# Kernel optimization log

Hardware: AMD Instinct MI355X
Metric: run time of the kernel (lower is better)

The kernel has to match this reference:

```python
import jax, jax.numpy as jnp
import numpy as np

H = 1024        # hidden_size
NH = 16         # num_heads
HD = H // NH    # head_dim
NS = 3          # num_strata


def setup_inputs() -> dict:
    key = jax.random.key(0)
    ks = jax.random.split(key, 12)
    s = 1.0 / np.sqrt(H)
    inp = {
        "hidden_states": jax.random.normal(ks[0], (2, 2048, H), dtype=jnp.float32),
        "Wq": jax.random.uniform(ks[1], (H, H), minval=-s, maxval=s, dtype=jnp.float32),
        "bq": jax.random.uniform(ks[2], (H,), minval=-s, maxval=s, dtype=jnp.float32),
        "Wk": jax.random.uniform(ks[3], (H, H), minval=-s, maxval=s, dtype=jnp.float32),
        "bk": jax.random.uniform(ks[4], (H,), minval=-s, maxval=s, dtype=jnp.float32),
        "Wv": jax.random.uniform(ks[5], (H, H), minval=-s, maxval=s, dtype=jnp.float32),
        "bv": jax.random.uniform(ks[6], (H,), minval=-s, maxval=s, dtype=jnp.float32),
        "Ws": jax.random.uniform(ks[7], (NS, H, H), minval=-s, maxval=s, dtype=jnp.float32),
        "bs": jax.random.uniform(ks[8], (NS, H), minval=-s, maxval=s, dtype=jnp.float32),
        "Wo": jax.random.uniform(ks[9], (H, H), minval=-s, maxval=s, dtype=jnp.float32),
        "bo": jax.random.uniform(ks[10], (H,), minval=-s, maxval=s, dtype=jnp.float32),
    }
    return inp


def reference(hidden_states, Wq, bq, Wk, bk, Wv, bv, Ws, bs, Wo, bo):
    B, S, _ = hidden_states.shape
    # torch nn.Linear: y = x @ W.T + b
    q = hidden_states @ Wq.T + bq
    k = hidden_states @ Wk.T + bk
    v = hidden_states @ Wv.T + bv
    # [B, NH, S, HD]
    q = q.reshape(B, S, NH, HD).transpose(0, 2, 1, 3)
    k = k.reshape(B, S, NH, HD).transpose(0, 2, 1, 3)
    v = v.reshape(B, S, NH, HD).transpose(0, 2, 1, 3)
    scores = jnp.einsum('bhqd,bhkd->bhqk', q, k) / jnp.sqrt(jnp.float32(HD))
    attn = jax.nn.softmax(scores, axis=-1)
    out = jnp.einsum('bhqk,bhkd->bhqd', attn, v)
    attn_output = out.transpose(0, 2, 1, 3).reshape(B, S, H)
    # stratum projections, averaged: [NS, B, S, H] -> mean over strata
    strata = jnp.einsum('bsh,ngh->nbsg', attn_output, Ws) + bs[:, None, None, :]
    enhanced = strata.mean(axis=0)
    output = enhanced @ Wo.T + bo
    return output
```

## Files before the change

### kernel.cpp

```cpp
#include <hip/hip_runtime.h>
#include <stdint.h>

typedef __attribute__((ext_vector_type(8))) short short8;
typedef __attribute__((ext_vector_type(4))) short short4v;
typedef __attribute__((ext_vector_type(4))) float f32x4;
typedef __attribute__((ext_vector_type(2))) unsigned int u32x2;
typedef unsigned int u32;
typedef const __attribute__((address_space(1))) u32* gas_ptr;
typedef __attribute__((address_space(3))) u32* las_ptr;

#define QSCALE 0.18033688011112042f

__device__ inline short f2bf(float x) {
    u32 u = __float_as_uint(x);
    u = u + 0x7FFFu + ((u >> 16) & 1u);
    return (short)(u >> 16);
}
__device__ inline void gload16(const void* g, const void* l) {
    __builtin_amdgcn_global_load_lds((gas_ptr)g, (las_ptr)l, 16, 0, 0);
}

__global__ __launch_bounds__(256) void prep(const float* __restrict__ X,
                                            const float* __restrict__ Wq,
                                            const float* __restrict__ Wk,
                                            const float* __restrict__ Wv,
                                            const float* __restrict__ Wo,
                                            const float* __restrict__ Ws,
                                            const float* __restrict__ bs,
                                            const float* __restrict__ bo,
                                            short* __restrict__ Xb,
                                            short* __restrict__ Wcat,
                                            short* __restrict__ Wob,
                                            short* __restrict__ WmT,
                                            float* __restrict__ bc) {
    __shared__ short T[64][65];
    const int tid = threadIdx.x;
    const int bid = blockIdx.x;
    if (bid < 8192) {
        const float* src;
        short* dst;
        int rel;
        if (bid < 4096)      { src = X;  dst = Xb;                rel = bid; }
        else if (bid < 5120) { src = Wq; dst = Wcat;              rel = bid - 4096; }
        else if (bid < 6144) { src = Wk; dst = Wcat + (1 << 20);  rel = bid - 5120; }
        else if (bid < 7168) { src = Wv; dst = Wcat + (2 << 20);  rel = bid - 6144; }
        else                 { src = Wo; dst = Wob;               rel = bid - 7168; }
        int i = (rel * 256 + tid) * 4;
        float4 v = *(const float4*)&src[i];
        short4v o;
        o[0] = f2bf(v.x); o[1] = f2bf(v.y); o[2] = f2bf(v.z); o[3] = f2bf(v.w);
        *(short4v*)&dst[i] = o;
    } else if (bid < 8448) {
        const int id = bid - 8192;
        const int gx = (id & 15) * 64, jy = (id >> 4) * 64;
        const int HH = 1 << 20;
        for (int e = tid; e < 4096; e += 256) {
            int j = e >> 6, g = e & 63;
            int idx = (jy + j) * 1024 + gx + g;
            float v = (Ws[idx] + Ws[idx + HH] + Ws[idx + 2 * HH]) * (1.0f / 3.0f);
            T[g][j] = f2bf(v);
        }
        __syncthreads();
        for (int e = tid; e < 4096; e += 256) {
            int g = e >> 6, j = e & 63;
            WmT[(long)(gx + g) * 1024 + jy + j] = T[g][j];
        }
    } else {
        const int lane = tid & 63;
        const int n = (bid - 8448) * 4 + (tid >> 6);
        float acc = 0.0f;
        for (int j0 = 0; j0 < 1024; j0 += 64) {
            int j = j0 + lane;
            float bm = (bs[j] + bs[j + 1024] + bs[j + 2048]) * (1.0f / 3.0f);
            acc += Wo[(long)n * 1024 + j] * bm;
        }
#pragma unroll
        for (int off = 1; off < 64; off <<= 1) acc += __shfl_xor(acc, off, 64);
        if (lane == 0) bc[n] = acc + bo[n];
    }
}

__global__ __launch_bounds__(256) void gemm_qkvwc(const short* __restrict__ Xb,
                                                  const short* __restrict__ Wcat,
                                                  const short* __restrict__ Wob,
                                                  const short* __restrict__ WmT,
                                                  const float* __restrict__ bq,
                                                  const float* __restrict__ bk,
                                                  const float* __restrict__ bv,
                                                  short* __restrict__ Qb,
                                                  short* __restrict__ Kb,
                                                  short* __restrict__ Vt,
                                                  short* __restrict__ Wc) {
    __shared__ short As[128 * 64];
    __shared__ short Bs[128 * 64];
    const int K = 1024;
    const int tid  = threadIdx.x;
    const int lane = tid & 63;
    const int wave = tid >> 6;
    const int quad = lane >> 4;
    const int l16  = lane & 15;
    const int bid = blockIdx.x;
    const short *A, *W;
    int m0, n0, sel;
    if (bid < 768) {
        m0 = (bid & 31) * 128;
        int t = bid >> 5;
        sel = t >> 3;
        n0 = (t & 7) * 128;
        A = Xb;
        W = Wcat + (long)sel * (1 << 20);
    } else {
        int w = bid - 768;
        sel = 3;
        m0 = (w >> 3) * 128;
        n0 = (w & 7) * 128;
        A = Wob;
        W = WmT;
    }
    const int wm = (wave >> 1) * 64;
    const int wn = (wave & 1) * 64;

    f32x4 acc[4][4] = {};
    const int sr = tid >> 3;
    const int scol = (((tid & 7) ^ (sr & 7)) << 3);
    const int fo_a = ((quad ^ (l16 & 7)) << 3);
    const int fo_b = (((4 + quad) ^ (l16 & 7)) << 3);

    for (int k0 = 0; k0 < K; k0 += 64) {
#pragma unroll
        for (int i = 0; i < 4; i++) {
            int r = i * 32 + sr;
            gload16(&A[(long)(m0 + r) * K + k0 + scol], &As[i * 2048 + wave * 512]);
            gload16(&W[(long)(n0 + r) * K + k0 + scol], &Bs[i * 2048 + wave * 512]);
        }
        __syncthreads();
        short8 bfr[4][2];
#pragma unroll
        for (int ni = 0; ni < 4; ni++) {
            const int row = wn + ni * 16 + l16;
            bfr[ni][0] = *(short8*)&Bs[row * 64 + fo_a];
            bfr[ni][1] = *(short8*)&Bs[row * 64 + fo_b];
        }
#pragma unroll
        for (int mi = 0; mi < 4; mi++) {
            const int row = wm + mi * 16 + l16;
            short8 af0 = *(short8*)&As[row * 64 + fo_a];
            short8 af1 = *(short8*)&As[row * 64 + fo_b];
#pragma unroll
            for (int ni = 0; ni < 4; ni++) {
                acc[mi][ni] = __builtin_amdgcn_mfma_f32_16x16x32_bf16(af0, bfr[ni][0],
                                                                      acc[mi][ni], 0, 0, 0);
                acc[mi][ni] = __builtin_amdgcn_mfma_f32_16x16x32_bf16(af1, bfr[ni][1],
                                                                      acc[mi][ni], 0, 0, 0);
            }
        }
        __syncthreads();
    }

#pragma unroll
    for (int mi = 0; mi < 4; mi++) {
#pragma unroll
        for (int ni = 0; ni < 4; ni++) {
            const int n = n0 + wn + ni * 16 + l16;
            const int mbase = m0 + wm + mi * 16 + quad * 4;
            float bv2 = 0.0f;
            if (sel == 0) bv2 = bq[n];
            else if (sel == 1) bv2 = bk[n];
            else if (sel == 2) bv2 = bv[n];
            if (sel == 2) {
                short4v pk;
#pragma unroll
                for (int r = 0; r < 4; r++) pk[r] = f2bf(acc[mi][ni][r] + bv2);
                long addr = ((long)(mbase >> 11) << 21) + (long)n * 2048 + (mbase & 2047);
                *(short4v*)&Vt[addr] = pk;
            } else if (sel == 0) {
#pragma unroll
                for (int r = 0; r < 4; r++)
                    Qb[(long)(mbase + r) * 1024 + n] = f2bf((acc[mi][ni][r] + bv2) * QSCALE);
            } else {
                short* C = (sel == 1) ? Kb : Wc;
#pragma unroll
                for (int r = 0; r < 4; r++)
                    C[(long)(mbase + r) * 1024 + n] = f2bf(acc[mi][ni][r] + bv2);
            }
        }
    }
}

__global__ __launch_bounds__(256) void attn_kernel(const short* __restrict__ Q,
                                                   const short* __restrict__ Kb,
                                                   const short* __restrict__ Vt,
                                                   short* __restrict__ O) {
    __shared__ short Ks[2][64 * 64];
    __shared__ short Vs[2][64 * 64];
    __shared__ short Ps[4][16 * 64];
    const int tid  = threadIdx.x;
    const int lane = tid & 63;
    const int wave = tid >> 6;
    const int quad = lane >> 4;
    const int l16  = lane & 15;
    const int q0 = blockIdx.x * 64;
    const int h  = blockIdx.y;
    const int b  = blockIdx.z;

    short8 qf0, qf1;
    {
        long base = (long)(b * 2048 + q0 + wave * 16 + l16) * 1024 + h * 64 + quad * 8;
        qf0 = *(const short8*)&Q[base];
        qf1 = *(const short8*)&Q[base + 32];
    }

    const int sr = tid >> 3;
    const int scol = (((tid & 7) ^ (sr & 7)) << 3);
    const short* Kp = Kb + (long)(b * 2048) * 1024 + h * 64;
    const short* Vp = Vt + ((long)b << 21) + (long)h * 64 * 2048;

    const int fo_a = ((quad ^ (l16 & 7)) << 3);
    const int fo_b = (((4 + quad) ^ (l16 & 7)) << 3);
    int po[4];
#pragma unroll
    for (int ni = 0; ni < 4; ni++)
        po[ni] = l16 * 64 + ((((2 * ni) + (quad >> 1)) ^ (l16 & 7)) << 3) + ((quad & 1) << 2);

    f32x4 o[4] = {};
    float lsum = 0.0f;

#pragma unroll
    for (int i = 0; i < 2; i++) {
        int r = i * 32 + sr;
        gload16(&Kp[(long)r * 1024 + scol], &Ks[0][i * 2048 + wave * 512]);
        gload16(&Vp[(long)r * 2048 + scol], &Vs[0][i * 2048 + wave * 512]);
    }
    __syncthreads();

    for (int kt = 0; kt < 32; kt++) {
        const int cur = kt & 1;
        if (kt < 31) {
            const int kbn = (kt + 1) * 64;
#pragma unroll
            for (int i = 0; i < 2; i++) {
                int r = i * 32 + sr;
                gload16(&Kp[(long)(kbn + r) * 1024 + scol], &Ks[cur ^ 1][i * 2048 + wave * 512]);
                gload16(&Vp[(long)r * 2048 + kbn + scol], &Vs[cur ^ 1][i * 2048 + wave * 512]);
            }
        }

#pragma unroll
        for (int ni = 0; ni < 4; ni++) {
            const int row = ni * 16 + l16;
            short8 ak0 = *(short8*)&Ks[cur][row * 64 + fo_a];
            short8 ak1 = *(short8*)&Ks[cur][row * 64 + fo_b];
            f32x4 s = {};
            s = __builtin_amdgcn_mfma_f32_16x16x32_bf16(ak0, qf0, s, 0, 0, 0);
            s = __builtin_amdgcn_mfma_f32_16x16x32_bf16(ak1, qf1, s, 0, 0, 0);
            float p0 = __builtin_amdgcn_exp2f(s[0]);
            float p1 = __builtin_amdgcn_exp2f(s[1]);
            float p2 = __builtin_amdgcn_exp2f(s[2]);
            float p3 = __builtin_amdgcn_exp2f(s[3]);
            lsum += (p0 + p1) + (p2 + p3);
            u32 a0 = __float_as_uint(p0) + 0x8000u;
            u32 a1 = __float_as_uint(p1) + 0x8000u;
            u32 a2 = __float_as_uint(p2) + 0x8000u;
            u32 a3 = __float_as_uint(p3) + 0x8000u;
            u32x2 w;
            w[0] = __builtin_amdgcn_perm(a1, a0, 0x07060302u);
            w[1] = __builtin_amdgcn_perm(a3, a2, 0x07060302u);
            *(u32x2*)&Ps[wave][po[ni]] = w;
        }

        short8 ap0 = *(short8*)&Ps[wave][l16 * 64 + fo_a];
        short8 ap1 = *(short8*)&Ps[wave][l16 * 64 + fo_b];
#pragma unroll
        for (int ni = 0; ni < 4; ni++) {
            const int row = ni * 16 + l16;
            short8 bv0 = *(short8*)&Vs[cur][row * 64 + fo_a];
            short8 bv1 = *(short8*)&Vs[cur][row * 64 + fo_b];
            o[ni] = __builtin_amdgcn_mfma_f32_16x16x32_bf16(ap0, bv0, o[ni], 0, 0, 0);
            o[ni] = __builtin_amdgcn_mfma_f32_16x16x32_bf16(ap1, bv1, o[ni], 0, 0, 0);
        }
        __syncthreads();
    }

    lsum += __shfl_xor(lsum, 16, 64);
    lsum += __shfl_xor(lsum, 32, 64);
#pragma unroll
    for (int r = 0; r < 4; r++) {
        const float tot = __shfl(lsum, quad * 4 + r, 64);
        const float inv = 1.0f / tot;
        const long row = (long)(b * 2048 + q0 + wave * 16 + quad * 4 + r) * 1024 + h * 64;
#pragma unroll
        for (int ni = 0; ni < 4; ni++)
            O[row + ni * 16 + l16] = f2bf(o[ni][r] * inv);
    }
}

__global__ __launch_bounds__(256) void gemm_final(const short* __restrict__ A,
                                                  const short* __restrict__ W,
                                                  const float* __restrict__ bias,
                                                  float* __restrict__ C) {
    __shared__ short As[64 * 64];
    __shared__ short Bs[128 * 64];
    const int K = 1024;
    const int tid  = threadIdx.x;
    const int lane = tid & 63;
    const int wave = tid >> 6;
    const int quad = lane >> 4;
    const int l16  = lane & 15;
    const int bid = blockIdx.x;
    const int m0 = (bid >> 3) * 64;
    const int n0 = (bid & 7) * 128;
    const int wm = (wave >> 1) * 32;
    const int wn = (wave & 1) * 64;

    f32x4 acc[2][4] = {};
    const int sr = tid >> 3;
    const int scol = (((tid & 7) ^ (sr & 7)) << 3);
    const int fo_a = ((quad ^ (l16 & 7)) << 3);
    const int fo_b = (((4 + quad) ^ (l16 & 7)) << 3);

    for (int k0 = 0; k0 < K; k0 += 64) {
#pragma unroll
        for (int i = 0; i < 2; i++) {
            int r = i * 32 + sr;
            gload16(&A[(long)(m0 + r) * K + k0 + scol], &As[i * 2048 + wave * 512]);
        }
#pragma unroll
        for (int i = 0; i < 4; i++) {
            int r = i * 32 + sr;
            gload16(&W[(long)(n0 + r) * K + k0 + scol], &Bs[i * 2048 + wave * 512]);
        }
        __syncthreads();
        short8 bfr[4][2];
#pragma unroll
        for (int ni = 0; ni < 4; ni++) {
            const int row = wn + ni * 16 + l16;
            bfr[ni][0] = *(short8*)&Bs[row * 64 + fo_a];
            bfr[ni][1] = *(short8*)&Bs[row * 64 + fo_b];
        }
#pragma unroll
        for (int mi = 0; mi < 2; mi++) {
            const int row = wm + mi * 16 + l16;
            short8 af0 = *(short8*)&As[row * 64 + fo_a];
            short8 af1 = *(short8*)&As[row * 64 + fo_b];
#pragma unroll
            for (int ni = 0; ni < 4; ni++) {
                acc[mi][ni] = __builtin_amdgcn_mfma_f32_16x16x32_bf16(af0, bfr[ni][0],
                                                                      acc[mi][ni], 0, 0, 0);
                acc[mi][ni] = __builtin_amdgcn_mfma_f32_16x16x32_bf16(af1, bfr[ni][1],
                                                                      acc[mi][ni], 0, 0, 0);
            }
        }
        __syncthreads();
    }

#pragma unroll
    for (int mi = 0; mi < 2; mi++) {
#pragma unroll
        for (int ni = 0; ni < 4; ni++) {
            const int n = n0 + wn + ni * 16 + l16;
            const float bv = bias[n];
            const int mbase = m0 + wm + mi * 16 + quad * 4;
#pragma unroll
            for (int r = 0; r < 4; r++)
                C[(long)(mbase + r) * 1024 + n] = acc[mi][ni][r] + bv;
        }
    }
}

extern "C" void kernel_launch(void* const* d_in, const int* in_sizes, int n_in,
                              void* d_out, int out_size, void* d_ws, size_t ws_size,
                              hipStream_t stream) {
    const float* X  = (const float*)d_in[0];
    const float* Wq = (const float*)d_in[1];
    const float* bq = (const float*)d_in[2];
    const float* Wk = (const float*)d_in[3];
    const float* bk = (const float*)d_in[4];
    const float* Wv = (const float*)d_in[5];
    const float* bv = (const float*)d_in[6];
    const float* Ws = (const float*)d_in[7];
    const float* bs = (const float*)d_in[8];
    const float* Wo = (const float*)d_in[9];
    const float* bo = (const float*)d_in[10];

    char* ws = (char*)d_ws;
    const long MB = 1 << 20;
    short* Xb   = (short*)(ws + 0 * MB);
    short* Wcat = (short*)(ws + 8 * MB);
    short* WmT  = (short*)(ws + 14 * MB);
    short* Wob  = (short*)(ws + 16 * MB);
    short* Wc   = (short*)(ws + 18 * MB);
    float* bc   = (float*)(ws + 20 * MB);
    short* Qb   = (short*)(ws + 21 * MB);
    short* Kbf  = (short*)(ws + 29 * MB);
    short* Vtb  = (short*)(ws + 37 * MB);
    short* AO   = Xb;

    dim3 bb(256);

    prep<<<dim3(8704), bb, 0, stream>>>(X, Wq, Wk, Wv, Wo, Ws, bs, bo,
                                        Xb, Wcat, Wob, WmT, bc);
    gemm_qkvwc<<<dim3(832), bb, 0, stream>>>(Xb, Wcat, Wob, WmT, bq, bk, bv,
                                             Qb, Kbf, Vtb, Wc);
    attn_kernel<<<dim3(32, 16, 2), bb, 0, stream>>>(Qb, Kbf, Vtb, AO);
    gemm_final<<<dim3(512), bb, 0, stream>>>(AO, Wc, bc, (float*)d_out);
}
```

Before: 231.4 us.

## Shrink QKV GEMM M-tile to 64 and single-buffer V in attention

The fused QKV/Wc GEMM now uses 64x128 output tiles instead of 128x128, doubling the grid from 832 to 1664 blocks and halving A-tile shared memory and accumulator registers. The goal is better occupancy and CU load balance, at the cost of reloading each weight tile from global memory twice as often. The attention kernel drops the V double buffer: V for the current tile is loaded at the start of each iteration, and the next K tile is prefetched after an added barrier. This halves V shared memory but adds a barrier per iteration and exposes the V load latency, which is no longer prefetched.

```diff
diff --git a/kernel.cpp b/kernel.cpp
--- a/kernel.cpp
+++ b/kernel.cpp
@@ -91,7 +91,7 @@
                                                   short* __restrict__ Kb,
                                                   short* __restrict__ Vt,
                                                   short* __restrict__ Wc) {
-    __shared__ short As[128 * 64];
+    __shared__ short As[64 * 64];
     __shared__ short Bs[128 * 64];
     const int K = 1024;
     const int tid  = threadIdx.x;
@@ -102,25 +102,25 @@
     const int bid = blockIdx.x;
     const short *A, *W;
     int m0, n0, sel;
-    if (bid < 768) {
-        m0 = (bid & 31) * 128;
-        int t = bid >> 5;
-        sel = t >> 3;
-        n0 = (t & 7) * 128;
+    if (bid < 1536) {
+        sel = bid >> 9;
+        int r = bid & 511;
+        m0 = (r >> 3) * 64;
+        n0 = (r & 7) * 128;
         A = Xb;
         W = Wcat + (long)sel * (1 << 20);
     } else {
-        int w = bid - 768;
+        int w = bid - 1536;
         sel = 3;
-        m0 = (w >> 3) * 128;
+        m0 = (w >> 3) * 64;
         n0 = (w & 7) * 128;
         A = Wob;
         W = WmT;
     }
-    const int wm = (wave >> 1) * 64;
+    const int wm = (wave >> 1) * 32;
     const int wn = (wave & 1) * 64;
 
-    f32x4 acc[4][4] = {};
+    f32x4 acc[2][4] = {};
     const int sr = tid >> 3;
     const int scol = (((tid & 7) ^ (sr & 7)) << 3);
     const int fo_a = ((quad ^ (l16 & 7)) << 3);
@@ -128,9 +128,13 @@
 
     for (int k0 = 0; k0 < K; k0 += 64) {
 #pragma unroll
+        for (int i = 0; i < 2; i++) {
+            int r = i * 32 + sr;
+            gload16(&A[(long)(m0 + r) * K + k0 + scol], &As[i * 2048 + wave * 512]);
+        }
+#pragma unroll
         for (int i = 0; i < 4; i++) {
             int r = i * 32 + sr;
-            gload16(&A[(long)(m0 + r) * K + k0 + scol], &As[i * 2048 + wave * 512]);
             gload16(&W[(long)(n0 + r) * K + k0 + scol], &Bs[i * 2048 + wave * 512]);
         }
         __syncthreads();
@@ -142,7 +146,7 @@
             bfr[ni][1] = *(short8*)&Bs[row * 64 + fo_b];
         }
 #pragma unroll
-        for (int mi = 0; mi < 4; mi++) {
+        for (int mi = 0; mi < 2; mi++) {
             const int row = wm + mi * 16 + l16;
             short8 af0 = *(short8*)&As[row * 64 + fo_a];
             short8 af1 = *(short8*)&As[row * 64 + fo_b];
@@ -158,7 +162,7 @@
     }
 
 #pragma unroll
-    for (int mi = 0; mi < 4; mi++) {
+    for (int mi = 0; mi < 2; mi++) {
 #pragma unroll
         for (int ni = 0; ni < 4; ni++) {
             const int n = n0 + wn + ni * 16 + l16;
@@ -192,7 +196,7 @@
                                                    const short* __restrict__ Vt,
                                                    short* __restrict__ O) {
     __shared__ short Ks[2][64 * 64];
-    __shared__ short Vs[2][64 * 64];
+    __shared__ short Vs[64 * 64];
     __shared__ short Ps[4][16 * 64];
     const int tid  = threadIdx.x;
     const int lane = tid & 63;
@@ -229,20 +233,17 @@
     for (int i = 0; i < 2; i++) {
         int r = i * 32 + sr;
         gload16(&Kp[(long)r * 1024 + scol], &Ks[0][i * 2048 + wave * 512]);
-        gload16(&Vp[(long)r * 2048 + scol], &Vs[0][i * 2048 + wave * 512]);
     }
     __syncthreads();
 
     for (int kt = 0; kt < 32; kt++) {
         const int cur = kt & 1;
-        if (kt < 31) {
-            const int kbn = (kt + 1) * 64;
-#pragma unroll
-            for (int i = 0; i < 2; i++) {
-                int r = i * 32 + sr;
-                gload16(&Kp[(long)(kbn + r) * 1024 + scol], &Ks[cur ^ 1][i * 2048 + wave * 512]);
-                gload16(&Vp[(long)r * 2048 + kbn + scol], &Vs[cur ^ 1][i * 2048 + wave * 512]);
-            }
+        const int kb = kt * 64;
+
+#pragma unroll
+        for (int i = 0; i < 2; i++) {
+            int r = i * 32 + sr;
+            gload16(&Vp[(long)r * 2048 + kb + scol], &Vs[i * 2048 + wave * 512]);
         }
 
 #pragma unroll
@@ -268,16 +269,29 @@
             *(u32x2*)&Ps[wave][po[ni]] = w;
         }
 
+        __syncthreads();
+
+        if (kt < 31) {
+            const int kbn = kb + 64;
+#pragma unroll
+            for (int i = 0; i < 2; i++) {
+                int r = i * 32 + sr;
+                gload16(&Kp[(long)(kbn + r) * 1024 + scol],
+                        &Ks[cur ^ 1][i * 2048 + wave * 512]);
+            }
+        }
+
         short8 ap0 = *(short8*)&Ps[wave][l16 * 64 + fo_a];
         short8 ap1 = *(short8*)&Ps[wave][l16 * 64 + fo_b];
 #pragma unroll
         for (int ni = 0; ni < 4; ni++) {
             const int row = ni * 16 + l16;
-            short8 bv0 = *(short8*)&Vs[cur][row * 64 + fo_a];
-            short8 bv1 = *(short8*)&Vs[cur][row * 64 + fo_b];
+            short8 bv0 = *(short8*)&Vs[row * 64 + fo_a];
+            short8 bv1 = *(short8*)&Vs[row * 64 + fo_b];
             o[ni] = __builtin_amdgcn_mfma_f32_16x16x32_bf16(ap0, bv0, o[ni], 0, 0, 0);
             o[ni] = __builtin_amdgcn_mfma_f32_16x16x32_bf16(ap1, bv1, o[ni], 0, 0, 0);
         }
+
         __syncthreads();
     }
 
@@ -399,8 +413,8 @@
 
     prep<<<dim3(8704), bb, 0, stream>>>(X, Wq, Wk, Wv, Wo, Ws, bs, bo,
                                         Xb, Wcat, Wob, WmT, bc);
-    gemm_qkvwc<<<dim3(832), bb, 0, stream>>>(Xb, Wcat, Wob, WmT, bq, bk, bv,
-                                             Qb, Kbf, Vtb, Wc);
+    gemm_qkvwc<<<dim3(1664), bb, 0, stream>>>(Xb, Wcat, Wob, WmT, bq, bk, bv,
+                                              Qb, Kbf, Vtb, Wc);
     attn_kernel<<<dim3(32, 16, 2), bb, 0, stream>>>(Qb, Kbf, Vtb, AO);
     gemm_final<<<dim3(512), bb, 0, stream>>>(AO, Wc, bc, (float*)d_out);
 }
```

After: 225.2 us. -2.7%, faster.
